# Performance work log

Hardware: AMD Instinct MI355X
Metric: run time of the kernel (lower is better)

The kernel has to match this reference:

```python
import jax, jax.numpy as jnp
import numpy as np

LEAK_RATE = 0.95


def setup_inputs() -> dict:
    key = jax.random.key(0)
    k1, k2, k3, k4 = jax.random.split(key, 4)
    B, S, I, H = 32, 2048, 512, 1024
    x = jax.random.normal(k1, (B, S, I), dtype=jnp.float32)
    # W_in: kaiming-uniform-like input projection (frozen)
    bound = 1.0 / np.sqrt(I)
    W_in = jax.random.uniform(k2, (H, I), dtype=jnp.float32, minval=-bound, maxval=bound)
    # W_res: sparse random matrix rescaled to spectral radius 1.2 (frozen)
    W = jax.random.normal(k3, (H, H), dtype=jnp.float32)
    mask = (jax.random.uniform(k4, (H, H)) > 0.1).astype(jnp.float32)  # sparsity=0.1
    W = W * mask
    eig = np.linalg.eigvals(np.asarray(W))
    radius = np.max(np.abs(eig)).astype(np.float32)
    W_res = W * (1.2 / (radius + 1e-8))
    return {"x": x, "W_in": W_in, "W_res": W_res}


def reference(x, W_in, W_res):
    # x: [B, S, I]; W_in: [H, I]; W_res: [H, H]
    B = x.shape[0]
    H = W_res.shape[0]
    # Precompute input projection for all timesteps (batched GEMM)
    u = jnp.einsum('bsi,hi->bsh', x, W_in)  # [B, S, H]
    init = jnp.zeros((B, H), dtype=x.dtype)

    def step(prev, u_t):
        new = jnp.tanh(u_t + prev @ W_res.T)
        new = LEAK_RATE * new + (1.0 - LEAK_RATE) * prev
        return new, new

    _, states = jax.lax.scan(step, init, jnp.swapaxes(u, 0, 1))  # [S, B, H]
    return jnp.swapaxes(states, 0, 1)  # [B, S, H]
```

## Files before the change

kernel.cpp:

```cpp
#include <hip/hip_runtime.h>
#include <cmath>

#define LEAK 0.95f
#define ILEAK 0.05f

typedef float f4 __attribute__((ext_vector_type(4)));
typedef short s8 __attribute__((ext_vector_type(8)));
typedef unsigned long long ull;

__global__ __launch_bounds__(256) void resv_gemm_uin(
    const float* __restrict__ A, const float* __restrict__ Bm,
    float* __restrict__ C, int M, int N, int K)
{
    __shared__ float As[16][68];
    __shared__ float Bs[16][68];
    const int tid = threadIdx.x;
    const int m0 = blockIdx.y * 64;
    const int n0 = blockIdx.x * 64;
    const int lm = tid >> 2;
    const int lk = (tid & 3) * 4;
    const int ty = tid >> 4;
    const int tx = tid & 15;

    float acc[4][4];
#pragma unroll
    for (int i = 0; i < 4; ++i)
#pragma unroll
        for (int j = 0; j < 4; ++j) acc[i][j] = 0.f;

    const float* Aptr = A + (size_t)(m0 + lm) * K + lk;
    const float* Bptr = Bm + (size_t)(n0 + lm) * K + lk;

    for (int k0 = 0; k0 < K; k0 += 16) {
        float4 av = *(const float4*)(Aptr + k0);
        float4 bv = *(const float4*)(Bptr + k0);
        __syncthreads();
        As[lk + 0][lm] = av.x; As[lk + 1][lm] = av.y;
        As[lk + 2][lm] = av.z; As[lk + 3][lm] = av.w;
        Bs[lk + 0][lm] = bv.x; Bs[lk + 1][lm] = bv.y;
        Bs[lk + 2][lm] = bv.z; Bs[lk + 3][lm] = bv.w;
        __syncthreads();
#pragma unroll
        for (int kk = 0; kk < 16; ++kk) {
            float4 a = *(const float4*)(&As[kk][ty * 4]);
            float4 b = *(const float4*)(&Bs[kk][tx * 4]);
            acc[0][0] += a.x * b.x; acc[0][1] += a.x * b.y; acc[0][2] += a.x * b.z; acc[0][3] += a.x * b.w;
            acc[1][0] += a.y * b.x; acc[1][1] += a.y * b.y; acc[1][2] += a.y * b.z; acc[1][3] += a.y * b.w;
            acc[2][0] += a.z * b.x; acc[2][1] += a.z * b.y; acc[2][2] += a.z * b.z; acc[2][3] += a.z * b.w;
            acc[3][0] += a.w * b.x; acc[3][1] += a.w * b.y; acc[3][2] += a.w * b.z; acc[3][3] += a.w * b.w;
        }
    }
    float* Cp = C + (size_t)(m0 + ty * 4) * N + n0 + tx * 4;
#pragma unroll
    for (int i = 0; i < 4; ++i) {
        float4 v = make_float4(acc[i][0], acc[i][1], acc[i][2], acc[i][3]);
        *(float4*)(Cp + (size_t)i * N) = v;
    }
}

__device__ __forceinline__ ushort f32_to_bf16_rne(float x) {
    unsigned u = __float_as_uint(x);
    return (ushort)((u + 0x7FFFu + ((u >> 16) & 1u)) >> 16);
}

__global__ __launch_bounds__(256, 1) void resv_recur(
    const float* __restrict__ Wres,
    float* __restrict__ out,
    ull* __restrict__ pairs)
{
    constexpr int H = 1024, S = 2048;
    extern __shared__ char smraw[];
    ushort* Bb  = (ushort*)smraw;
    float*  uL  = (float*)(smraw + 8448);
    float*  red = (float*)(smraw + 8448 + 16384);

    const int tid = threadIdx.x;
    const int g  = blockIdx.x & 7;
    const int r  = blockIdx.x >> 3;
    const int h0 = r * 32;
    const int b0 = g * 4;

    const int w  = tid >> 6;
    const int l  = tid & 63;
    const int lg = l >> 4;
    const int lc = l & 15;

    s8 Afrag[16];
#pragma unroll
    for (int m = 0; m < 2; ++m)
#pragma unroll
        for (int kt = 0; kt < 8; ++kt) {
            const float* wp = Wres + (size_t)(h0 + m * 16 + lc) * H
                            + (w * 256 + kt * 32 + lg * 8);
            s8 a;
#pragma unroll
            for (int j = 0; j < 8; ++j) a[j] = (short)f32_to_bf16_rne(wp[j]);
            Afrag[m * 8 + kt] = a;
        }

    const int fb  = tid & 3;
    const int frw = tid >> 2;
    float pv = 0.f;

    const ushort* bbase = Bb + (size_t)(lc & 3) * 1040 + w * 256 + lg * 8;

    for (int t = 0; t < S; ++t) {
        if ((t & 15) == 0) {
            float* uB = uL + ((t >> 4) & 1) * 2048;
            for (int c = tid; c < 512; c += 256) {
                int rw4 = c & 7, b = (c >> 3) & 3, tt = c >> 5;
                const float4* src =
                    (const float4*)(out + ((size_t)(b0 + b) * S + (t + tt)) * H + h0);
                ((float4*)uB)[(tt * 4 + b) * 8 + rw4] = src[rw4];
            }
        }
        {
            const ull* src = pairs + ((size_t)((t & 1) * 8 + g)) * 4096;
            const unsigned tgt = (unsigned)t;
            ull v[16];
            for (;;) {
                ull s0 = __hip_atomic_load(src + 0 * 256 + tid, __ATOMIC_RELAXED,
                                           __HIP_MEMORY_SCOPE_AGENT);
                ull s1 = __hip_atomic_load(src + 5 * 256 + tid, __ATOMIC_RELAXED,
                                           __HIP_MEMORY_SCOPE_AGENT);
                ull s2 = __hip_atomic_load(src + 10 * 256 + tid, __ATOMIC_RELAXED,
                                           __HIP_MEMORY_SCOPE_AGENT);
                ull s3 = __hip_atomic_load(src + 15 * 256 + tid, __ATOMIC_RELAXED,
                                           __HIP_MEMORY_SCOPE_AGENT);
                int ok = ((unsigned)(s0 >> 32) == tgt) & ((unsigned)(s1 >> 32) == tgt)
                       & ((unsigned)(s2 >> 32) == tgt) & ((unsigned)(s3 >> 32) == tgt);
                if (__all(ok)) { v[0] = s0; v[5] = s1; v[10] = s2; v[15] = s3; break; }
            }
            for (;;) {
                int ok = 1;
#pragma unroll
                for (int c = 0; c < 16; ++c) {
                    if (c == 0 || c == 5 || c == 10 || c == 15) continue;
                    v[c] = __hip_atomic_load(src + c * 256 + tid, __ATOMIC_RELAXED,
                                             __HIP_MEMORY_SCOPE_AGENT);
                    ok &= ((unsigned)(v[c] >> 32) == tgt);
                }
                if (__all(ok)) break;
            }
#pragma unroll
            for (int c = 0; c < 16; ++c) {
                int n = c * 256 + tid;
                Bb[(n & 3) * 1040 + (n >> 2)] =
                    f32_to_bf16_rne(__uint_as_float((unsigned)v[c]));
            }
        }
        __syncthreads();

        f4 c0 = (f4)(0.f), c1 = (f4)(0.f);
#pragma unroll
        for (int kt = 0; kt < 8; ++kt) {
            s8 bf = *(const s8*)(bbase + kt * 32);
            c0 = __builtin_amdgcn_mfma_f32_16x16x32_bf16(Afrag[kt],     bf, c0, 0, 0, 0);
            c1 = __builtin_amdgcn_mfma_f32_16x16x32_bf16(Afrag[8 + kt], bf, c1, 0, 0, 0);
        }
        if (lc < 4) {
#pragma unroll
            for (int j = 0; j < 4; ++j) {
                red[(w * 32 + lg * 4 + j) * 4 + lc]      = c0[j];
                red[(w * 32 + 16 + lg * 4 + j) * 4 + lc] = c1[j];
            }
        }
        __syncthreads();

        if (tid < 128) {
            float sum = red[(0 * 32 + frw) * 4 + fb] + red[(1 * 32 + frw) * 4 + fb]
                      + red[(2 * 32 + frw) * 4 + fb] + red[(3 * 32 + frw) * 4 + fb];
            float uv = uL[((t >> 4) & 1) * 2048 + (((t & 15) * 4 + fb) << 5) + frw];
            float ns = LEAK * tanhf(uv + sum) + ILEAK * pv;
            pv = ns;
            ull pk = ((ull)(unsigned)(t + 1) << 32) | (ull)__float_as_uint(ns);
            __hip_atomic_store(
                pairs + ((size_t)(((t + 1) & 1) * 8 + g)) * 4096 + h0 * 4 + tid,
                pk, __ATOMIC_RELAXED, __HIP_MEMORY_SCOPE_AGENT);
            out[((size_t)(b0 + fb) * S + t) * H + h0 + frw] = ns;
        }
        __syncthreads();
    }
}

extern "C" void kernel_launch(void* const* d_in, const int* in_sizes, int n_in,
                              void* d_out, int out_size, void* d_ws, size_t ws_size,
                              hipStream_t stream)
{
    const float* x    = (const float*)d_in[0];
    const float* Win  = (const float*)d_in[1];
    const float* Wres = (const float*)d_in[2];
    float* out = (float*)d_out;

    ull* pairs = (ull*)d_ws;

    hipMemsetAsync(d_ws, 0, 524288, stream);

    dim3 gemm_grid(1024 / 64, 65536 / 64);
    resv_gemm_uin<<<gemm_grid, 256, 0, stream>>>(x, Win, out, 65536, 1024, 512);

    constexpr int kLds = 96 * 1024;
    hipFuncSetAttribute((const void*)resv_recur,
                        hipFuncAttributeMaxDynamicSharedMemorySize, kLds);
    resv_recur<<<dim3(256), dim3(256), kLds, stream>>>(Wres, out, pairs);
}
```

Before: 5.205 ms.

## Pack bf16 state pairs with 16-bit tags and double-buffer LDS to drop a barrier

Each recurrence step now publishes two bf16 hidden values per 64-bit word, each carrying a 16-bit step tag, instead of one fp32 value with a 32-bit tag. This halves the global polling and exchange traffic between blocks, and each thread loads 8 words per step instead of 16. The B operand and reduction buffers in LDS are double-buffered by step parity, which lets the trailing __syncthreads be removed. In exchange, the bf16 rounding moves to the producer, a cross-lane shuffle is added, and the tag is cut to 16 bits, which still fits the 2048 steps.

```diff
diff --git a/kernel.cpp b/kernel.cpp
--- a/kernel.cpp
+++ b/kernel.cpp
@@ -58,9 +58,9 @@
     }
 }
 
-__device__ __forceinline__ ushort f32_to_bf16_rne(float x) {
+__device__ __forceinline__ unsigned f32_to_bf16_rne(float x) {
     unsigned u = __float_as_uint(x);
-    return (ushort)((u + 0x7FFFu + ((u >> 16) & 1u)) >> 16);
+    return (u + 0x7FFFu + ((u >> 16) & 1u)) >> 16;
 }
 
 __global__ __launch_bounds__(256, 1) void resv_recur(
@@ -71,8 +71,8 @@
     constexpr int H = 1024, S = 2048;
     extern __shared__ char smraw[];
     ushort* Bb  = (ushort*)smraw;
-    float*  uL  = (float*)(smraw + 8448);
-    float*  red = (float*)(smraw + 8448 + 16384);
+    float*  uL  = (float*)(smraw + 16640);
+    float*  red = (float*)(smraw + 16640 + 16384);
 
     const int tid = threadIdx.x;
     const int g  = blockIdx.x & 7;
@@ -102,9 +102,8 @@
     const int frw = tid >> 2;
     float pv = 0.f;
 
-    const ushort* bbase = Bb + (size_t)(lc & 3) * 1040 + w * 256 + lg * 8;
-
     for (int t = 0; t < S; ++t) {
+        const int p = t & 1;
         if ((t & 15) == 0) {
             float* uB = uL + ((t >> 4) & 1) * 2048;
             for (int c = tid; c < 512; c += 256) {
@@ -115,71 +114,72 @@
             }
         }
         {
-            const ull* src = pairs + ((size_t)((t & 1) * 8 + g)) * 4096;
-            const unsigned tgt = (unsigned)t;
-            ull v[16];
+            const ull* src = pairs + ((size_t)(p * 8 + g)) * 2048;
+            const ull tg = (ull)(unsigned short)t;
+            const ull tpat = (tg << 48) | (tg << 16);
+            ull v[8];
             for (;;) {
-                ull s0 = __hip_atomic_load(src + 0 * 256 + tid, __ATOMIC_RELAXED,
-                                           __HIP_MEMORY_SCOPE_AGENT);
-                ull s1 = __hip_atomic_load(src + 5 * 256 + tid, __ATOMIC_RELAXED,
-                                           __HIP_MEMORY_SCOPE_AGENT);
-                ull s2 = __hip_atomic_load(src + 10 * 256 + tid, __ATOMIC_RELAXED,
-                                           __HIP_MEMORY_SCOPE_AGENT);
-                ull s3 = __hip_atomic_load(src + 15 * 256 + tid, __ATOMIC_RELAXED,
-                                           __HIP_MEMORY_SCOPE_AGENT);
-                int ok = ((unsigned)(s0 >> 32) == tgt) & ((unsigned)(s1 >> 32) == tgt)
-                       & ((unsigned)(s2 >> 32) == tgt) & ((unsigned)(s3 >> 32) == tgt);
-                if (__all(ok)) { v[0] = s0; v[5] = s1; v[10] = s2; v[15] = s3; break; }
-            }
-            for (;;) {
-                int ok = 1;
-#pragma unroll
-                for (int c = 0; c < 16; ++c) {
-                    if (c == 0 || c == 5 || c == 10 || c == 15) continue;
+#pragma unroll
+                for (int c = 0; c < 8; ++c)
                     v[c] = __hip_atomic_load(src + c * 256 + tid, __ATOMIC_RELAXED,
                                              __HIP_MEMORY_SCOPE_AGENT);
-                    ok &= ((unsigned)(v[c] >> 32) == tgt);
+                int ok = 1;
+#pragma unroll
+                for (int c = 0; c < 8; ++c)
+                    ok &= ((v[c] & 0xFFFF0000FFFF0000ull) == tpat);
+                if (__all(ok)) break;
+            }
+            uint* bw = (uint*)(Bb + (size_t)p * 4160);
+#pragma unroll
+            for (int c = 0; c < 8; ++c) {
+                int idx = c * 256 + tid;
+                uint word = (uint)(v[c] & 0xFFFFu)
+                          | ((uint)((v[c] >> 32) & 0xFFFFu) << 16);
+                bw[(idx >> 9) * 520 + (idx & 511)] = word;
+            }
+        }
+        __syncthreads();
+
+        {
+            const ushort* bbase = Bb + (size_t)p * 4160 + (lc & 3) * 1040
+                                + w * 256 + lg * 8;
+            f4 c0 = (f4)(0.f), c1 = (f4)(0.f);
+#pragma unroll
+            for (int kt = 0; kt < 8; ++kt) {
+                s8 bf = *(const s8*)(bbase + kt * 32);
+                c0 = __builtin_amdgcn_mfma_f32_16x16x32_bf16(Afrag[kt],     bf, c0, 0, 0, 0);
+                c1 = __builtin_amdgcn_mfma_f32_16x16x32_bf16(Afrag[8 + kt], bf, c1, 0, 0, 0);
+            }
+            float* redB = red + p * 512;
+            if (lc < 4) {
+#pragma unroll
+                for (int j = 0; j < 4; ++j) {
+                    redB[(w * 32 + lg * 4 + j) * 4 + lc]      = c0[j];
+                    redB[(w * 32 + 16 + lg * 4 + j) * 4 + lc] = c1[j];
                 }
-                if (__all(ok)) break;
-            }
-#pragma unroll
-            for (int c = 0; c < 16; ++c) {
-                int n = c * 256 + tid;
-                Bb[(n & 3) * 1040 + (n >> 2)] =
-                    f32_to_bf16_rne(__uint_as_float((unsigned)v[c]));
-            }
-        }
-        __syncthreads();
-
-        f4 c0 = (f4)(0.f), c1 = (f4)(0.f);
-#pragma unroll
-        for (int kt = 0; kt < 8; ++kt) {
-            s8 bf = *(const s8*)(bbase + kt * 32);
-            c0 = __builtin_amdgcn_mfma_f32_16x16x32_bf16(Afrag[kt],     bf, c0, 0, 0, 0);
-            c1 = __builtin_amdgcn_mfma_f32_16x16x32_bf16(Afrag[8 + kt], bf, c1, 0, 0, 0);
-        }
-        if (lc < 4) {
-#pragma unroll
-            for (int j = 0; j < 4; ++j) {
-                red[(w * 32 + lg * 4 + j) * 4 + lc]      = c0[j];
-                red[(w * 32 + 16 + lg * 4 + j) * 4 + lc] = c1[j];
             }
         }
         __syncthreads();
 
         if (tid < 128) {
-            float sum = red[(0 * 32 + frw) * 4 + fb] + red[(1 * 32 + frw) * 4 + fb]
-                      + red[(2 * 32 + frw) * 4 + fb] + red[(3 * 32 + frw) * 4 + fb];
+            const float* redB = red + p * 512;
+            float sum = redB[(0 * 32 + frw) * 4 + fb] + redB[(1 * 32 + frw) * 4 + fb]
+                      + redB[(2 * 32 + frw) * 4 + fb] + redB[(3 * 32 + frw) * 4 + fb];
             float uv = uL[((t >> 4) & 1) * 2048 + (((t & 15) * 4 + fb) << 5) + frw];
             float ns = LEAK * tanhf(uv + sum) + ILEAK * pv;
             pv = ns;
-            ull pk = ((ull)(unsigned)(t + 1) << 32) | (ull)__float_as_uint(ns);
-            __hip_atomic_store(
-                pairs + ((size_t)(((t + 1) & 1) * 8 + g)) * 4096 + h0 * 4 + tid,
-                pk, __ATOMIC_RELAXED, __HIP_MEMORY_SCOPE_AGENT);
+            unsigned nb = f32_to_bf16_rne(ns);
+            unsigned hb = (unsigned)__shfl_xor((int)nb, 4, 64);
+            if ((tid & 4) == 0) {
+                ull T = (ull)(unsigned short)(t + 1);
+                ull pk = (T << 48) | ((ull)hb << 32) | (T << 16) | (ull)nb;
+                __hip_atomic_store(
+                    pairs + ((size_t)(((t + 1) & 1) * 8 + g)) * 2048
+                          + fb * 512 + (h0 >> 1) + (frw >> 1),
+                    pk, __ATOMIC_RELAXED, __HIP_MEMORY_SCOPE_AGENT);
+            }
             out[((size_t)(b0 + fb) * S + t) * H + h0 + frw] = ns;
         }
-        __syncthreads();
     }
 }
 
@@ -194,7 +194,7 @@
 
     ull* pairs = (ull*)d_ws;
 
-    hipMemsetAsync(d_ws, 0, 524288, stream);
+    hipMemsetAsync(d_ws, 0, 262144, stream);
 
     dim3 gemm_grid(1024 / 64, 65536 / 64);
     resv_gemm_uin<<<gemm_grid, 256, 0, stream>>>(x, Win, out, 65536, 1024, 512);
```

New measurement: 6.686 ms. 1.28x slower.
